# Kernel optimization log

Hardware: AMD Instinct MI355X
Metric: run time of the kernel (lower is better)

## Reference

```python
import jax, jax.numpy as jnp
import numpy as np

R = 59        # num relations (58 + 1)
D = 128       # node_feat_size
K = 16        # neighbors_sample


def _lstm(windows, Wk, Wr, b):
    # windows: [N, T, F]; standard Keras LSTM (gate order i, f, g, o).
    N = windows.shape[0]
    z_in = jnp.einsum('ntf,fh->nth', windows, Wk) + b        # [N, T, 4D]
    z_in = jnp.swapaxes(z_in, 0, 1)                          # [T, N, 4D]

    def step(carry, zt):
        h, c = carry
        z = zt + h @ Wr
        i, f, g, o = jnp.split(z, 4, axis=-1)
        i = jax.nn.sigmoid(i)
        f = jax.nn.sigmoid(f)
        g = jnp.tanh(g)
        o = jax.nn.sigmoid(o)
        c = f * c + i * g
        h = o * jnp.tanh(c)
        return (h, c), None

    h0 = jnp.zeros((N, D), windows.dtype)
    (h, _), _ = jax.lax.scan(step, (h0, h0), z_in)
    return h                                                 # [N, D]


def setup_inputs() -> dict:
    key = jax.random.key(0)
    ks = jax.random.split(key, 12)
    N, T, F = 1024, 32, 10
    s = 0.05
    return {
        'windows': jax.random.normal(ks[0], (N, T, F), jnp.float32),
        'neighbors': jax.random.randint(ks[1], (R, N, K), 0, N + 1, jnp.int32),
        'lstm_kernel': jax.random.normal(ks[2], (F, 4 * D), jnp.float32) * s,
        'lstm_recurrent': jax.random.normal(ks[3], (D, 4 * D), jnp.float32) * s,
        'lstm_bias': jax.random.normal(ks[4], (4 * D,), jnp.float32) * s,
        'W_state': jax.random.normal(ks[5], (R, 2 * D + R), jnp.float32) * s,
        'b_state': jax.random.normal(ks[6], (R,), jnp.float32) * s,
        'W_relattn': jax.random.normal(ks[7], (2 * D + R,), jnp.float32) * s,
        'b_relattn': jax.random.normal(ks[8], (1,), jnp.float32) * s,
        'W_pred': jax.random.normal(ks[9], (D, 3), jnp.float32) * s,
        'b_pred': jax.random.normal(ks[10], (3,), jnp.float32) * s,
    }


def reference(windows, neighbors, lstm_kernel, lstm_recurrent, lstm_bias,
              W_state, b_state, W_relattn, b_relattn, W_pred, b_pred):
    cur = _lstm(windows, lstm_kernel, lstm_recurrent, lstm_bias)    # [N, D]
    feats = jnp.concatenate([jnp.zeros((1, D), cur.dtype), cur], 0)  # [N+1, D]

    # --- per-relation state attention ---
    # Dense(1) on concat(cur, nbr, onehot(rel)) splits into three dot products.
    Wc = W_state[:, :D]            # [R, D]
    Wn = W_state[:, D:2 * D]       # [R, D]
    Wrr = W_state[:, 2 * D:]       # [R, R]; onehot picks the diagonal
    rel_term = jnp.diagonal(Wrr) + b_state                  # [R]
    cur_term = cur @ Wc.T                                    # [N, R]
    nbr_proj = feats @ Wn.T                                  # [N+1, R]
    # gather the scalar neighbor projection per relation: [R, N, K]
    nbr_term = jax.vmap(lambda idx, p: p[idx])(neighbors, nbr_proj.T)
    scores = jax.nn.relu(cur_term.T[:, :, None] + nbr_term
                         + rel_term[:, None, None])          # [R, N, K]
    w = jax.nn.softmax(scores, axis=-1)
    nbr_feats = feats[neighbors]                             # [R, N, K, D]
    rel_reps = jnp.einsum('rnk,rnkd->rnd', w, nbr_feats)     # [R, N, D]

    # --- relation attention ---
    wc = W_relattn[:D]
    wn = W_relattn[D:2 * D]
    wr = W_relattn[2 * D:]                                   # [R]
    s2 = jax.nn.relu((cur @ wc)[None, :]
                     + jnp.einsum('rnd,d->rn', rel_reps, wn)
                     + wr[:, None] + b_relattn[0])           # [R, N]
    aw = jax.nn.softmax(s2, axis=0)
    rel_agg = jnp.einsum('rn,rnd->nd', aw, rel_reps)         # [N, D]
    updated = cur + rel_agg

    logits = updated @ W_pred + b_pred                       # [N, 3]
    predictions = jax.nn.softmax(logits, axis=-1)
    return logits, predictions, updated
```

## Files before the change

### kernel.cpp

```cpp
#include <hip/hip_runtime.h>
#include <hip/hip_bf16.h>

constexpr int R  = 59;
constexpr int D  = 128;
constexpr int NK = 16;
constexpr int N  = 1024;
constexpr int T  = 32;
constexpr int F  = 10;
constexpr int H4 = 512;
constexpr int WSTRIDE = 2*D + R;

typedef __attribute__((ext_vector_type(8))) short short8;
typedef __attribute__((ext_vector_type(4))) float f32x4;

__device__ __forceinline__ float sigm(float x) {
  return __builtin_amdgcn_rcpf(1.0f + __expf(-x));
}
__device__ __forceinline__ float tanh_(float x) {
  return 2.0f * __builtin_amdgcn_rcpf(1.0f + __expf(-2.0f * x)) - 1.0f;
}
__device__ __forceinline__ ushort f2bf(float f) {
  unsigned u = __float_as_uint(f);
  u += 0x7FFF + ((u >> 16) & 1);
  return (ushort)(u >> 16);
}

__device__ int g_detect_f32(const void* windows) {
  const __hip_bfloat16* p = (const __hip_bfloat16*)windows;
  int weird = 0;
  for (int i = 0; i < 128; ++i) {
    float v = __bfloat162float(p[i]);
    float a = fabsf(v);
    if (!(a <= 100.0f) || (v != 0.0f && a < 1e-8f)) ++weird;
  }
  return weird > 8;
}

__device__ __forceinline__ float rdsrc(const void* p, int i, int isf32) {
  return isf32 ? ((const float*)p)[i]
               : __bfloat162float(((const __hip_bfloat16*)p)[i]);
}

struct CvtA {
  const void* small[6];
  int soff[7];
  const void* win;
  const void* wk;
  const void* wr;
  const void* bias;
};

__global__ __launch_bounds__(256) void convert_kernel(
    CvtA a, float* __restrict__ csm, float* __restrict__ wt,
    ushort* __restrict__ bpk, ushort* __restrict__ xwin,
    int* __restrict__ flag_out)
{
  __shared__ int sflag;
  if (threadIdx.x == 0) sflag = g_detect_f32(a.win);
  __syncthreads();
  const int isf32 = sflag;
  if (blockIdx.x == 0 && threadIdx.x == 0) flag_out[0] = isf32;
  const int gid = blockIdx.x * 256 + threadIdx.x;
  const int stride = gridDim.x * 256;

  for (int i = gid; i < a.soff[6]; i += stride) {
    int t = 0;
    while (t < 5 && i >= a.soff[t + 1]) ++t;
    csm[i] = rdsrc(a.small[t], i - a.soff[t], isf32);
  }
  for (int i = gid; i < 128 * 128; i += stride) {
    const int d = i >> 7, j = i & 127;
    float v = 0.0f;
    if (j < 59)        v = rdsrc(a.small[0], j * WSTRIDE + D + d, isf32);
    else if (j < 118)  v = rdsrc(a.small[0], (j - 59) * WSTRIDE + d, isf32);
    else if (j == 118) v = rdsrc(a.small[2], d, isf32);
    wt[i] = v;
  }
  for (int fi = gid; fi < 10240; fi += stride) {
    const int l  = fi & 63;
    const int kf = (fi >> 6) % 5;
    const int g  = ((fi >> 6) / 5) & 3;
    const int w  = (fi >> 6) / 20;
    const int col = g * 128 + w * 16 + (l & 15);
    const int q   = l >> 4;
#pragma unroll
    for (int j = 0; j < 8; ++j) {
      const int k = q * 8 + j;
      float v;
      if (kf < 4)      v = rdsrc(a.wr, (kf * 32 + k) * H4 + col, isf32);
      else if (k < 10) v = rdsrc(a.wk, k * H4 + col, isf32);
      else if (k == 10) v = rdsrc(a.bias, col, isf32);
      else             v = 0.0f;
      bpk[fi * 8 + j] = f2bf(v);
    }
  }
  for (int i = gid; i < N * T * 16; i += stride) {
    const int f = i & 15, nt = i >> 4;
    float v = (f < F) ? rdsrc(a.win, nt * F + f, isf32)
                      : (f == 10 ? 1.0f : 0.0f);
    xwin[i] = f2bf(v);
  }
}

__global__ __launch_bounds__(512)
__attribute__((amdgpu_waves_per_eu(2, 2)))
void lstm_kernel(const ushort* __restrict__ bpk, const ushort* __restrict__ xwin,
                 float* __restrict__ feats, ushort* __restrict__ fb16)
{
  const int tid = threadIdx.x;
  const int w   = tid >> 6;
  const int l   = tid & 63;
  const int n0  = blockIdx.x * 16;

  __shared__ ushort hbuf[2][16 * 136];
  __shared__ ushort xfrag[T * 64 * 8];

  if (blockIdx.x == 0 && tid < D) { feats[tid] = 0.0f; fb16[tid] = 0; }

  for (int p = tid; p < T * 64; p += 512) {
    const int t = p >> 6, ll = p & 63, s = ll & 15, q = ll >> 4;
    *(short8*)&xfrag[p * 8] = *(const short8*)&xwin[(n0 + s) * (T * 16) + t * 16 + q * 8];
  }
  for (int i = tid; i < 2 * 16 * 136; i += 512) ((ushort*)hbuf)[i] = 0;

  short8 B[4][5];
#pragma unroll
  for (int g = 0; g < 4; ++g)
#pragma unroll
    for (int kf = 0; kf < 5; ++kf)
      B[g][kf] = *(const short8*)&bpk[((((w * 4 + g) * 5 + kf) * 64) + l) * 8];

  f32x4 c4 = {0.f, 0.f, 0.f, 0.f};
  float hreg[4];
  const int lq    = l >> 4;
  const int krow0 = lq * 8;
  const int srow0 = lq * 4;
  const int col_d = w * 16 + (l & 15);

  __syncthreads();

  for (int t = 0; t < T; ++t) {
    const ushort* hb = hbuf[t & 1];
    short8 A[5];
#pragma unroll
    for (int kf = 0; kf < 4; ++kf)
      A[kf] = *(const short8*)(hb + (l & 15) * 136 + kf * 32 + krow0);
    A[4] = *(const short8*)(xfrag + (t * 64 + l) * 8);

    f32x4 acc[4];
#pragma unroll
    for (int g = 0; g < 4; ++g) {
      acc[g] = (f32x4){0.f, 0.f, 0.f, 0.f};
#pragma unroll
      for (int kf = 0; kf < 5; ++kf)
        acc[g] = __builtin_amdgcn_mfma_f32_16x16x32_bf16(A[kf], B[g][kf], acc[g], 0, 0, 0);
    }

    ushort* hw = hbuf[(t + 1) & 1];
#pragma unroll
    for (int r = 0; r < 4; ++r) {
      const float i_ = sigm(acc[0][r]);
      const float f_ = sigm(acc[1][r]);
      const float g_ = tanh_(acc[2][r]);
      const float o_ = sigm(acc[3][r]);
      c4[r]   = f_ * c4[r] + i_ * g_;
      hreg[r] = o_ * tanh_(c4[r]);
      hw[(srow0 + r) * 136 + col_d] = f2bf(hreg[r]);
    }
    __syncthreads();
  }

#pragma unroll
  for (int r = 0; r < 4; ++r) {
    feats[(n0 + srow0 + r + 1) * D + col_d] = hreg[r];
    fb16 [(n0 + srow0 + r + 1) * D + col_d] = f2bf(hreg[r]);
  }
}

__global__ __launch_bounds__(128) void proj_kernel(
    const float* __restrict__ feats, const float* __restrict__ wt,
    float* __restrict__ cur_term, float* __restrict__ nbr_proj,
    float* __restrict__ curwc)
{
  const int m = blockIdx.x;
  const int j = threadIdx.x;
  __shared__ float frow[128];
  frow[j] = feats[m * D + j];
  __syncthreads();

  float acc = 0.0f;
#pragma unroll 8
  for (int d = 0; d < 128; ++d)
    acc = fmaf(frow[d], wt[d * 128 + j], acc);

  if (j < 59) nbr_proj[m * R + j] = acc;
  else if (m >= 1) {
    if (j < 118)       cur_term[(m - 1) * R + (j - 59)] = acc;
    else if (j == 118) curwc[m - 1] = acc;
  }
}

__device__ __forceinline__ void store_out(void* out, int i, float v, int outf32) {
  if (outf32) ((float*)out)[i] = v;
  else        ((__hip_bfloat16*)out)[i] = __float2bfloat16(v);
}

__global__ __launch_bounds__(256) void attn_kernel(
    const float* __restrict__ feats, const ushort* __restrict__ fb16,
    const int* __restrict__ neighbors,
    const float* __restrict__ W_state, const float* __restrict__ b_state,
    const float* __restrict__ W_relattn, const float* __restrict__ b_relattn,
    const float* __restrict__ W_pred, const float* __restrict__ b_pred,
    const float* __restrict__ cur_term, const float* __restrict__ nbr_proj,
    const float* __restrict__ curwc, const int* __restrict__ flagp,
    void* __restrict__ out)
{
  const int n   = blockIdx.x;
  const int tid = threadIdx.x;

  __shared__ float  rr[R * 132];
  __shared__ int    idx_lds[R * NK];
  __shared__ float  w_lds[NK * 60];
  __shared__ float  s2part[16 * 68];
  __shared__ float  wn_lds[D];
  __shared__ float  ct_lds[R];
  __shared__ float  rt_lds[R];
  __shared__ float  s2_lds[R];
  __shared__ float  aw_lds[R];
  __shared__ float  upd_lds[D];
  __shared__ int    sflag;

  if (tid == 0) sflag = flagp[0];
  if (tid < R) {
    ct_lds[tid] = cur_term[n * R + tid];
    rt_lds[tid] = W_state[tid * WSTRIDE + 2 * D + tid] + b_state[tid];
  }
  if (tid >= 128 && tid < 256) wn_lds[tid - 128] = W_relattn[D + (tid - 128)];
  for (int i = tid; i < R * NK; i += 256) {
    const int r = i >> 4, k = i & 15;
    idx_lds[i] = neighbors[(r * N + n) * NK + k];
  }
  __syncthreads();
  const int outf32 = sflag;

  for (int i = tid; i < R * NK; i += 256) {
    const int r = i >> 4, k = i & 15;
    float s = ct_lds[r] + nbr_proj[idx_lds[i] * R + r] + rt_lds[r];
    w_lds[k * 60 + r] = fmaxf(s, 0.0f);
  }
  __syncthreads();

  if (tid < R) {
    float mx = 0.0f;
#pragma unroll
    for (int k = 0; k < NK; ++k) mx = fmaxf(mx, w_lds[k * 60 + tid]);
    float sum = 0.0f;
    float e[NK];
#pragma unroll
    for (int k = 0; k < NK; ++k) {
      e[k] = __expf(w_lds[k * 60 + tid] - mx);
      sum += e[k];
    }
    const float inv = __builtin_amdgcn_rcpf(sum);
#pragma unroll
    for (int k = 0; k < NK; ++k) w_lds[k * 60 + tid] = e[k] * inv;
  }
  __syncthreads();

  {
    const int d8 = tid & 15;
    const int rp = tid >> 4;
    for (int r = rp; r < R; r += 16) {
      float acc[8];
#pragma unroll
      for (int j = 0; j < 8; ++j) acc[j] = 0.0f;
#pragma unroll
      for (int k = 0; k < NK; ++k) {
        const int m = idx_lds[r * NK + k];
        const uint4 v = *(const uint4*)&fb16[m * D + d8 * 8];
        const float wv = w_lds[k * 60 + r];
        acc[0] = fmaf(wv, __uint_as_float(v.x << 16),          acc[0]);
        acc[1] = fmaf(wv, __uint_as_float(v.x & 0xffff0000u),  acc[1]);
        acc[2] = fmaf(wv, __uint_as_float(v.y << 16),          acc[2]);
        acc[3] = fmaf(wv, __uint_as_float(v.y & 0xffff0000u),  acc[3]);
        acc[4] = fmaf(wv, __uint_as_float(v.z << 16),          acc[4]);
        acc[5] = fmaf(wv, __uint_as_float(v.z & 0xffff0000u),  acc[5]);
        acc[6] = fmaf(wv, __uint_as_float(v.w << 16),          acc[6]);
        acc[7] = fmaf(wv, __uint_as_float(v.w & 0xffff0000u),  acc[7]);
      }
      *(float4*)&rr[r * 132 + d8 * 8]     = (float4){acc[0], acc[1], acc[2], acc[3]};
      *(float4*)&rr[r * 132 + d8 * 8 + 4] = (float4){acc[4], acc[5], acc[6], acc[7]};
      float p = 0.0f;
#pragma unroll
      for (int j = 0; j < 8; ++j) p = fmaf(acc[j], wn_lds[d8 * 8 + j], p);
      s2part[d8 * 68 + r] = p;
    }
  }
  __syncthreads();

  if (tid < R) {
    float dot = 0.0f;
#pragma unroll
    for (int q = 0; q < 16; ++q) dot += s2part[q * 68 + tid];
    float v = curwc[n] + dot + W_relattn[2 * D + tid] + b_relattn[0];
    s2_lds[tid] = fmaxf(v, 0.0f);
  }
  __syncthreads();

  if (tid < 64) {
    float v = (tid < R) ? s2_lds[tid] : -1e30f;
    float mx = v;
    for (int off = 32; off; off >>= 1) mx = fmaxf(mx, __shfl_xor(mx, off));
    float e = (tid < R) ? __expf(v - mx) : 0.0f;
    float sum = e;
    for (int off = 32; off; off >>= 1) sum += __shfl_xor(sum, off);
    if (tid < R) aw_lds[tid] = e / sum;
  }
  __syncthreads();

  if (tid < D) {
    float agg = 0.0f;
    for (int r = 0; r < R; ++r) agg = fmaf(aw_lds[r], rr[r * 132 + tid], agg);
    const float upd = feats[(n + 1) * D + tid] + agg;
    store_out(out, 2 * 3 * N + n * D + tid, upd, outf32);
    upd_lds[tid] = upd;
  }
  __syncthreads();

  if (tid < 64) {
    float p[3];
#pragma unroll
    for (int j = 0; j < 3; ++j) {
      float v = upd_lds[tid] * W_pred[tid * 3 + j] +
                upd_lds[tid + 64] * W_pred[(tid + 64) * 3 + j];
      for (int off = 32; off; off >>= 1) v += __shfl_xor(v, off);
      p[j] = v + b_pred[j];
    }
    if (tid == 0) {
      const float mx = fmaxf(p[0], fmaxf(p[1], p[2]));
      const float e0 = __expf(p[0] - mx), e1 = __expf(p[1] - mx), e2 = __expf(p[2] - mx);
      const float s = e0 + e1 + e2;
      store_out(out, n * 3 + 0, p[0], outf32);
      store_out(out, n * 3 + 1, p[1], outf32);
      store_out(out, n * 3 + 2, p[2], outf32);
      store_out(out, 3 * N + n * 3 + 0, e0 / s, outf32);
      store_out(out, 3 * N + n * 3 + 1, e1 / s, outf32);
      store_out(out, 3 * N + n * 3 + 2, e2 / s, outf32);
    }
  }
}

extern "C" void kernel_launch(void* const* d_in, const int* in_sizes, int n_in,
                              void* d_out, int out_size, void* d_ws, size_t ws_size,
                              hipStream_t stream)
{
  const int* neighbors = (const int*)d_in[1];
  float* ws = (float*)d_ws;

  CvtA ca;
  {
    constexpr int SS[6] = {18585, 59, 315, 1, 384, 3};
    int off = 0;
    for (int i = 0; i < 6; ++i) { ca.small[i] = d_in[5 + i]; ca.soff[i] = off; off += SS[i]; }
    ca.soff[6] = off;
    ca.win  = d_in[0];
    ca.wk   = d_in[2];
    ca.wr   = d_in[3];
    ca.bias = d_in[4];
  }

  float*  csm      = ws;
  float*  wtpack   = csm + 19360;
  float*  feats    = wtpack + 16384;
  float*  cur_term = feats + 131200;
  float*  nbr_proj = cur_term + 60416;
  float*  curwc    = nbr_proj + 60480;
  int*    flagp    = (int*)(curwc + 1024);
  ushort* bpk      = (ushort*)(curwc + 1040);
  ushort* xwin     = bpk + 81920;
  ushort* fb16     = xwin + 524288;

  const float* c_Wstate = csm;
  const float* c_bstate = csm + 18585;
  const float* c_Wrel   = csm + 18644;
  const float* c_brel   = csm + 18959;
  const float* c_Wpred  = csm + 18960;
  const float* c_bpred  = csm + 19344;

  convert_kernel<<<512, 256, 0, stream>>>(ca, csm, wtpack, bpk, xwin, flagp);
  lstm_kernel<<<N / 16, 512, 0, stream>>>(bpk, xwin, feats, fb16);
  proj_kernel<<<N + 1, 128, 0, stream>>>(feats, wtpack, cur_term, nbr_proj, curwc);
  attn_kernel<<<N, 256, 0, stream>>>(feats, fb16, neighbors, c_Wstate, c_bstate, c_Wrel,
                                     c_brel, c_Wpred, c_bpred,
                                     cur_term, nbr_proj, curwc, flagp, d_out);
}
```

Baseline: 78.09 us.

## Fuse window conversion into LSTM load and store relation reps as bf16

Removes the staging xwin buffer. The LSTM kernel now reads the raw windows directly and converts them to bf16 fragments in shared memory, which drops a global write and read pass and shrinks the convert grid. The attention kernel also stores per-relation representations in LDS as bf16 instead of fp32, halving LDS use to raise occupancy. This costs extra precision loss in the aggregation and uncoalesced strided reads of the raw windows inside the LSTM prologue.

```diff
diff --git a/kernel.cpp b/kernel.cpp
--- a/kernel.cpp
+++ b/kernel.cpp
@@ -24,6 +24,9 @@
   u += 0x7FFF + ((u >> 16) & 1);
   return (ushort)(u >> 16);
 }
+__device__ __forceinline__ float bf2f(ushort u) {
+  return __uint_as_float(((unsigned)u) << 16);
+}
 
 __device__ int g_detect_f32(const void* windows) {
   const __hip_bfloat16* p = (const __hip_bfloat16*)windows;
@@ -52,8 +55,7 @@
 
 __global__ __launch_bounds__(256) void convert_kernel(
     CvtA a, float* __restrict__ csm, float* __restrict__ wt,
-    ushort* __restrict__ bpk, ushort* __restrict__ xwin,
-    int* __restrict__ flag_out)
+    ushort* __restrict__ bpk, int* __restrict__ flag_out)
 {
   __shared__ int sflag;
   if (threadIdx.x == 0) sflag = g_detect_f32(a.win);
@@ -94,17 +96,12 @@
       bpk[fi * 8 + j] = f2bf(v);
     }
   }
-  for (int i = gid; i < N * T * 16; i += stride) {
-    const int f = i & 15, nt = i >> 4;
-    float v = (f < F) ? rdsrc(a.win, nt * F + f, isf32)
-                      : (f == 10 ? 1.0f : 0.0f);
-    xwin[i] = f2bf(v);
-  }
 }
 
 __global__ __launch_bounds__(512)
 __attribute__((amdgpu_waves_per_eu(2, 2)))
-void lstm_kernel(const ushort* __restrict__ bpk, const ushort* __restrict__ xwin,
+void lstm_kernel(const ushort* __restrict__ bpk, const void* __restrict__ win_raw,
+                 const int* __restrict__ flagp,
                  float* __restrict__ feats, ushort* __restrict__ fb16)
 {
   const int tid = threadIdx.x;
@@ -117,9 +114,18 @@
 
   if (blockIdx.x == 0 && tid < D) { feats[tid] = 0.0f; fb16[tid] = 0; }
 
+  const int isf32 = flagp[0];
   for (int p = tid; p < T * 64; p += 512) {
     const int t = p >> 6, ll = p & 63, s = ll & 15, q = ll >> 4;
-    *(short8*)&xfrag[p * 8] = *(const short8*)&xwin[(n0 + s) * (T * 16) + t * 16 + q * 8];
+    short8 pk;
+#pragma unroll
+    for (int j = 0; j < 8; ++j) {
+      const int f = q * 8 + j;
+      float v = (f < F) ? rdsrc(win_raw, (n0 + s) * (T * F) + t * F + f, isf32)
+                        : (f == 10 ? 1.0f : 0.0f);
+      pk[j] = (short)f2bf(v);
+    }
+    *(short8*)&xfrag[p * 8] = pk;
   }
   for (int i = tid; i < 2 * 16 * 136; i += 512) ((ushort*)hbuf)[i] = 0;
 
@@ -218,7 +224,7 @@
   const int n   = blockIdx.x;
   const int tid = threadIdx.x;
 
-  __shared__ float  rr[R * 132];
+  __shared__ ushort rr[R * 136];
   __shared__ int    idx_lds[R * NK];
   __shared__ float  w_lds[NK * 60];
   __shared__ float  s2part[16 * 68];
@@ -288,8 +294,10 @@
         acc[6] = fmaf(wv, __uint_as_float(v.w << 16),          acc[6]);
         acc[7] = fmaf(wv, __uint_as_float(v.w & 0xffff0000u),  acc[7]);
       }
-      *(float4*)&rr[r * 132 + d8 * 8]     = (float4){acc[0], acc[1], acc[2], acc[3]};
-      *(float4*)&rr[r * 132 + d8 * 8 + 4] = (float4){acc[4], acc[5], acc[6], acc[7]};
+      short8 pk;
+#pragma unroll
+      for (int j = 0; j < 8; ++j) pk[j] = (short)f2bf(acc[j]);
+      *(short8*)&rr[r * 136 + d8 * 8] = pk;
       float p = 0.0f;
 #pragma unroll
       for (int j = 0; j < 8; ++j) p = fmaf(acc[j], wn_lds[d8 * 8 + j], p);
@@ -320,7 +328,7 @@
 
   if (tid < D) {
     float agg = 0.0f;
-    for (int r = 0; r < R; ++r) agg = fmaf(aw_lds[r], rr[r * 132 + tid], agg);
+    for (int r = 0; r < R; ++r) agg = fmaf(aw_lds[r], bf2f(rr[r * 136 + tid]), agg);
     const float upd = feats[(n + 1) * D + tid] + agg;
     store_out(out, 2 * 3 * N + n * D + tid, upd, outf32);
     upd_lds[tid] = upd;
@@ -377,8 +385,7 @@
   float*  curwc    = nbr_proj + 60480;
   int*    flagp    = (int*)(curwc + 1024);
   ushort* bpk      = (ushort*)(curwc + 1040);
-  ushort* xwin     = bpk + 81920;
-  ushort* fb16     = xwin + 524288;
+  ushort* fb16     = bpk + 81920;
 
   const float* c_Wstate = csm;
   const float* c_bstate = csm + 18585;
@@ -387,8 +394,8 @@
   const float* c_Wpred  = csm + 18960;
   const float* c_bpred  = csm + 19344;
 
-  convert_kernel<<<512, 256, 0, stream>>>(ca, csm, wtpack, bpk, xwin, flagp);
-  lstm_kernel<<<N / 16, 512, 0, stream>>>(bpk, xwin, feats, fb16);
+  convert_kernel<<<256, 256, 0, stream>>>(ca, csm, wtpack, bpk, flagp);
+  lstm_kernel<<<N / 16, 512, 0, stream>>>(bpk, d_in[0], flagp, feats, fb16);
   proj_kernel<<<N + 1, 128, 0, stream>>>(feats, wtpack, cur_term, nbr_proj, curwc);
   attn_kernel<<<N, 256, 0, stream>>>(feats, fb16, neighbors, c_Wstate, c_bstate, c_Wrel,
                                      c_brel, c_Wpred, c_bpred,
```

Result: faster. 75.22 us (median of 2 runs) (-3.7%).
